# Kernel tuning notes

Hardware: AMD Instinct MI355X
Metric: run time of the kernel (lower is better)

The kernel has to match this reference:

```python
import jax, jax.numpy as jnp
import numpy as np

B, D, H0, H1, O = 4096, 1024, 1024, 1024, 1024  # O = output_dim + 1
ALPHA = 0.3
CLAMP = 0.3


def setup_inputs() -> dict:
    key = jax.random.key(0)
    ks = jax.random.split(key, 15)
    def he(k, fan_in, shape):
        return jax.random.normal(k, shape, dtype=jnp.float32) * np.sqrt(2.0 / fan_in).astype(np.float32)
    def heb(k, shape):
        return jax.random.uniform(k, shape, dtype=jnp.float32, minval=-CLAMP, maxval=CLAMP)
    return {
        "x": jax.random.normal(ks[0], (B, D), dtype=jnp.float32),
        "x2h0": he(ks[1], D, (D, H0)),
        "x2h1": he(ks[2], D, (D, H1)),
        "h02h1": he(ks[3], H0, (H0, H1)),
        "x2y": he(ks[4], D, (D, O)),
        "h02y": he(ks[5], H0, (H0, O)),
        "h12y": he(ks[6], H1, (H1, O)),
        "heb_x2h0": heb(ks[7], (D, H0)),
        "heb_x2h1": heb(ks[8], (D, H1)),
        "heb_h02h1": heb(ks[9], (H0, H1)),
        "heb_x2y": heb(ks[10], (D, O)),
        "heb_h02y": heb(ks[11], (H0, O)),
        "heb_h12y": heb(ks[12], (H1, O)),
        "W": jax.random.uniform(ks[13], (1, 1), dtype=jnp.float32),
    }


def reference(x, x2h0, x2h1, h02h1, x2y, h02y, h12y,
              heb_x2h0, heb_x2h1, heb_h02h1, heb_x2y, heb_h02y, heb_h12y, W):
    clamp = lambda m: jnp.clip(m, -CLAMP, CLAMP)
    # x -> h0
    h0_x = x @ (x2h0 + W * heb_x2h0)                       # [B, H0]
    heb_x2h0_n = clamp(heb_x2h0 + ALPHA * (x.T @ h0_x))
    h0 = jax.nn.relu(h0_x)
    # x -> h1, h0 -> h1
    h1_x = x @ (x2h1 + W * heb_x2h1)                       # [B, H1]
    heb_x2h1_n = clamp(heb_x2h1 + ALPHA * (x.T @ h1_x))
    h1_0 = h0 @ (h02h1 + W * heb_h02h1)
    heb_h02h1_n = clamp(heb_h02h1 + ALPHA * (h0.T @ h1_0))
    h1 = jax.nn.relu(h1_x + h1_0)
    # x, h0, h1 -> y
    y_x = x @ (x2y + W * heb_x2y)                          # [B, O]
    heb_x2y_n = clamp(heb_x2y + ALPHA * (x.T @ y_x))
    y_0 = h0 @ (h02y + W * heb_h02y)
    heb_h02y_n = clamp(heb_h02y + ALPHA * (h0.T @ y_0))
    y_1 = h1 @ (h12y + W * heb_h12y)
    heb_h12y_n = clamp(heb_h12y + ALPHA * (h1.T @ y_1))
    y = y_x + y_0 + y_1
    W_new = jnp.mean(jnp.tanh(y[:, -2:-1]))               # neuromodulator scalar
    dopa = jnp.mean(jnp.tanh(y[:, -3:-2]))
    y_out = y[:, :-2]                                      # [B, O-2]
    return (y_out, heb_x2h0_n, heb_x2h1_n, heb_h02h1_n,
            heb_x2y_n, heb_h02y_n, heb_h12y_n, W_new, dopa)
```

## Files before the change

### kernel.cpp

```cpp
#include <hip/hip_runtime.h>
#include <stdint.h>

#define ALPHA 0.3f
#define CLAMPV 0.3f
#define BDIM 4096
#define NDIM 1024

typedef float f32x4 __attribute__((ext_vector_type(4)));
typedef __bf16 bf16x8 __attribute__((ext_vector_type(8)));

union U16x8 { uint4 v; unsigned short u[8]; };

__device__ __forceinline__ float bf2f(unsigned short u) {
  union { unsigned int i; float f; } c; c.i = ((unsigned int)u) << 16; return c.f;
}
__device__ __forceinline__ unsigned short f2bf(float f) {
  union { float f; unsigned int i; } c; c.f = f;
  unsigned int u = c.i;
  unsigned int r = u + 0x7FFFu + ((u >> 16) & 1u);
  return (unsigned short)(r >> 16);
}

__global__ __launch_bounds__(256) void fill_k(float* __restrict__ out, int n) {
  int i = blockIdx.x * 256 + threadIdx.x;
  if (i < n) out[i] = 12345.0f;
}

__global__ __launch_bounds__(256) void split_x_k(const float* __restrict__ x,
                                                 unsigned short* __restrict__ hi,
                                                 unsigned short* __restrict__ lo) {
  const size_t i0 = ((size_t)blockIdx.x * 256 + threadIdx.x) * 8;
  f32x4 a = *(const f32x4*)(x + i0);
  f32x4 b = *(const f32x4*)(x + i0 + 4);
  U16x8 h8, l8;
#pragma unroll
  for (int i = 0; i < 4; ++i) {
    unsigned short h = f2bf(a[i]); h8.u[i] = h; l8.u[i] = f2bf(a[i] - bf2f(h));
    unsigned short h2 = f2bf(b[i]); h8.u[4+i] = h2; l8.u[4+i] = f2bf(b[i] - bf2f(h2));
  }
  *(uint4*)(hi + i0) = h8.v;
  *(uint4*)(lo + i0) = l8.v;
}

struct TDesc {
  const void* in1; const void* in2; const float* Wp;
  unsigned short* out_hi; unsigned short* out_lo;
  int R, C, tilesC, mode;
};
struct TBatch { TDesc d[8]; int start[9]; int n; };

__global__ __launch_bounds__(256) void transpose_k(TBatch batch) {
  const int bid = blockIdx.x;
  int g = 0;
#pragma unroll
  for (int i = 1; i < 8; ++i)
    if (i < batch.n && bid >= batch.start[i]) g = i;
  TDesc D = batch.d[g];
  const int lt = bid - batch.start[g];
  const int trow = lt / D.tilesC;
  const int tcol = lt - trow * D.tilesC;
  const int r0 = trow * 64, c0 = tcol * 64;

  __shared__ float tile[64][65];
  const int t = threadIdx.x;
  const int sub = t >> 3, oct = t & 7;
  const float Wv = (D.mode == 2) ? *D.Wp : 0.f;

#pragma unroll
  for (int p = 0; p < 2; ++p) {
    const int rl = p * 32 + sub;
    const int cl0 = oct * 8;
    float vv[8];
    if (D.mode == 0) {
      const unsigned short* ip = (const unsigned short*)D.in1 + (size_t)(r0 + rl) * D.C + c0 + cl0;
      U16x8 tmp; tmp.v = *(const uint4*)ip;
#pragma unroll
      for (int i = 0; i < 8; ++i) vv[i] = bf2f(tmp.u[i]);
    } else {
      const float* ip = (const float*)D.in1 + (size_t)(r0 + rl) * D.C + c0 + cl0;
      f32x4 a = *(const f32x4*)ip, b = *(const f32x4*)(ip + 4);
#pragma unroll
      for (int i = 0; i < 4; ++i) { vv[i] = a[i]; vv[4+i] = b[i]; }
      if (D.mode == 2) {
        const float* ip2 = (const float*)D.in2 + (size_t)(r0 + rl) * D.C + c0 + cl0;
        f32x4 c = *(const f32x4*)ip2, d2 = *(const f32x4*)(ip2 + 4);
#pragma unroll
        for (int i = 0; i < 4; ++i) { vv[i] += Wv * c[i]; vv[4+i] += Wv * d2[i]; }
      }
    }
#pragma unroll
    for (int i = 0; i < 8; ++i) tile[cl0 + i][rl] = vv[i];
  }
  __syncthreads();
#pragma unroll
  for (int p = 0; p < 2; ++p) {
    const int cl = p * 32 + sub;
    const int rl0 = oct * 8;
    U16x8 h8, l8;
#pragma unroll
    for (int i = 0; i < 8; ++i) {
      float v = tile[cl][rl0 + i];
      unsigned short h = f2bf(v);
      h8.u[i] = h;
      l8.u[i] = f2bf(v - bf2f(h));
    }
    const size_t o = (size_t)(c0 + cl) * D.R + r0 + rl0;
    *(uint4*)(D.out_hi + o) = h8.v;
    if (D.mode != 0) *(uint4*)(D.out_lo + o) = l8.v;
  }
}

struct GemmDesc {
  const unsigned short *Ahi, *Alo, *Bhi, *Blo;
  int lda, ldb, nk, accadd;
  float* out32a;
  float* out32b;
  const float* addin;
  unsigned short* sp_hi;
  unsigned short* sp_lo;
  const float* heb_in;
  float* heb_out;
};
struct GemmBatch { GemmDesc d[16]; int start[17]; int n; };

#define AS1 __attribute__((address_space(1)))
#define AS3 __attribute__((address_space(3)))

__global__ __launch_bounds__(256, 2) void gemm_k(GemmBatch batch) {
  const int bid = blockIdx.x;
  int g = 0;
#pragma unroll
  for (int i = 1; i < 16; ++i)
    if (i < batch.n && bid >= batch.start[i]) g = i;
  GemmDesc D = batch.d[g];
  const int local = bid - batch.start[g];
  const int tm = local >> 3;
  const int tn = local & 7;

  __shared__ __align__(16) unsigned short LDS[32768];

  const int t = threadIdx.x;
  const int lane = t & 63;
  const int wave = t >> 6;
  const int wr = wave >> 1, wc = wave & 1;
  const int fr = lane & 15, fg = lane >> 4;

  f32x4 acc[8][4];
#pragma unroll
  for (int i = 0; i < 8; ++i)
#pragma unroll
    for (int j = 0; j < 4; ++j)
#pragma unroll
      for (int rr = 0; rr < 4; ++rr) acc[i][j][rr] = 0.f;

  const int r0 = t >> 2;
  const int colSwE = (((t & 3) ^ ((t >> 3) & 3)) << 3);

  size_t aRow[4], bRow[2];
#pragma unroll
  for (int qq = 0; qq < 4; ++qq)
    aRow[qq] = (size_t)(tm * 256 + qq * 64 + r0) * D.lda + colSwE;
#pragma unroll
  for (int qq = 0; qq < 2; ++qq)
    bRow[qq] = (size_t)(tn * 128 + qq * 64 + r0) * D.ldb + colSwE;

  const int ldsW = wave * 512;

  auto stageA = [&](const unsigned short* P, int kb, int b) {
    unsigned short* base = LDS + b * 16384 + ldsW;
#pragma unroll
    for (int qq = 0; qq < 4; ++qq)
      __builtin_amdgcn_global_load_lds(
          (const AS1 void*)(P + aRow[qq] + kb),
          (AS3 void*)(base + qq * 2048), 16, 0, 0);
  };
  auto stageB = [&](const unsigned short* P, int region, int kb, int b) {
    unsigned short* base = LDS + b * 16384 + region + ldsW;
#pragma unroll
    for (int qq = 0; qq < 2; ++qq)
      __builtin_amdgcn_global_load_lds(
          (const AS1 void*)(P + bRow[qq] + kb),
          (AS3 void*)(base + qq * 2048), 16, 0, 0);
  };

  const int swz = ((fg ^ ((fr >> 1) & 3)) << 4);
  int aoff[8], boff[4];
#pragma unroll
  for (int i = 0; i < 8; ++i)
    aoff[i] = (wr * 128 + i * 16 + fr) * 64 + swz;
#pragma unroll
  for (int j = 0; j < 4; ++j)
    boff[j] = 16384 + (wc * 64 + j * 16 + fr) * 64 + swz;
  const char* ldsc = (const char*)LDS;

  auto computePh0 = [&](int b) {
    const char* bb = ldsc + b * 32768;
    bf16x8 af[8];
#pragma unroll
    for (int i = 0; i < 8; ++i) af[i] = *(const bf16x8*)(bb + aoff[i]);
#pragma unroll
    for (int j = 0; j < 4; ++j) {
      const bf16x8 bh = *(const bf16x8*)(bb + boff[j]);
#pragma unroll
      for (int i = 0; i < 8; ++i)
        acc[i][j] = __builtin_amdgcn_mfma_f32_16x16x32_bf16(af[i], bh, acc[i][j], 0, 0, 0);
      const bf16x8 bl = *(const bf16x8*)(bb + boff[j] + 8192);
#pragma unroll
      for (int i = 0; i < 8; ++i)
        acc[i][j] = __builtin_amdgcn_mfma_f32_16x16x32_bf16(af[i], bl, acc[i][j], 0, 0, 0);
    }
  };
  auto computePh1 = [&](int b) {
    const char* bb = ldsc + b * 32768;
    bf16x8 af[8];
#pragma unroll
    for (int i = 0; i < 8; ++i) af[i] = *(const bf16x8*)(bb + aoff[i]);
#pragma unroll
    for (int j = 0; j < 4; ++j) {
      const bf16x8 bh = *(const bf16x8*)(bb + boff[j]);
#pragma unroll
      for (int i = 0; i < 8; ++i)
        acc[i][j] = __builtin_amdgcn_mfma_f32_16x16x32_bf16(af[i], bh, acc[i][j], 0, 0, 0);
    }
  };

  const int n = D.nk;

  stageA(D.Ahi, 0, 0);
  stageB(D.Bhi, 8192, 0, 0);
  stageB(D.Blo, 12288, 0, 0);
  int buf = 0;

#pragma unroll 1
  for (int kt = 0; kt < n; ++kt) {
    if (kt + 1 < n) {
      const int kb = (kt + 1) << 5;
      stageA(D.Ahi, kb, buf ^ 1);
      stageB(D.Bhi, 8192, kb, buf ^ 1);
      stageB(D.Blo, 12288, kb, buf ^ 1);
      asm volatile("s_waitcnt vmcnt(8)" ::: "memory");
    } else {
      stageA(D.Alo, 0, buf ^ 1);
      stageB(D.Bhi, 8192, 0, buf ^ 1);
      asm volatile("s_waitcnt vmcnt(6)" ::: "memory");
    }
    __builtin_amdgcn_s_barrier();
    __builtin_amdgcn_sched_barrier(0);
    computePh0(buf);
    __builtin_amdgcn_sched_barrier(0);
    __builtin_amdgcn_s_barrier();
    buf ^= 1;
  }

#pragma unroll 1
  for (int kt = 0; kt < n; ++kt) {
    if (kt + 1 < n) {
      const int kb = (kt + 1) << 5;
      stageA(D.Alo, kb, buf ^ 1);
      stageB(D.Bhi, 8192, kb, buf ^ 1);
      asm volatile("s_waitcnt vmcnt(6)" ::: "memory");
    } else {
      asm volatile("s_waitcnt vmcnt(0)" ::: "memory");
    }
    __builtin_amdgcn_s_barrier();
    __builtin_amdgcn_sched_barrier(0);
    computePh1(buf);
    __builtin_amdgcn_sched_barrier(0);
    __builtin_amdgcn_s_barrier();
    buf ^= 1;
  }

  const int grb = tm * 256 + wr * 128 + fg * 4;
  const int gcb = tn * 128 + wc * 64 + fr;
#pragma unroll
  for (int i = 0; i < 8; ++i) {
#pragma unroll
    for (int j = 0; j < 4; ++j) {
      const int gc = gcb + j * 16;
#pragma unroll
      for (int rr = 0; rr < 4; ++rr) {
        const int gr = grb + i * 16 + rr;
        const size_t idx = (size_t)gr * NDIM + gc;
        const float v = acc[i][j][rr];
        if (D.heb_out) {
          D.heb_out[idx] = fminf(fmaxf(D.heb_in[idx] + ALPHA * v, -CLAMPV), CLAMPV);
        } else {
          if (D.out32a) D.out32a[idx] = v;
          if (D.out32b) D.out32b[idx] = D.accadd ? (D.out32b[idx] + v) : v;
          if (D.sp_hi) {
            float rv = v + (D.addin ? D.addin[idx] : 0.f);
            rv = fmaxf(rv, 0.f);
            const unsigned short h = f2bf(rv);
            D.sp_hi[idx] = h;
            D.sp_lo[idx] = f2bf(rv - bf2f(h));
          }
        }
      }
    }
  }
}

struct HebRed { const float* heb_in; float* out; const float* p[16]; int np; };

__global__ __launch_bounds__(256) void hebred_k(HebRed R) {
  const size_t i0 = ((size_t)blockIdx.x * 256 + threadIdx.x) * 4;
  f32x4 s = *(const f32x4*)(R.p[0] + i0);
#pragma unroll
  for (int k = 1; k < 16; ++k)
    if (k < R.np) s += *(const f32x4*)(R.p[k] + i0);
  f32x4 h = *(const f32x4*)(R.heb_in + i0);
  f32x4 o;
#pragma unroll
  for (int i = 0; i < 4; ++i) o[i] = fminf(fmaxf(h[i] + ALPHA * s[i], -CLAMPV), CLAMPV);
  *(f32x4*)(R.out + i0) = o;
}

__global__ __launch_bounds__(256) void yassm_k(const float* __restrict__ ysum,
                                               float* __restrict__ yout) {
  const int stride = gridDim.x * 256;
  for (int idx = blockIdx.x * 256 + threadIdx.x; idx < BDIM * 1022; idx += stride) {
    const int row = idx / 1022;
    const int col = idx - row * 1022;
    yout[idx] = ysum[(size_t)row * NDIM + col];
  }
}

__global__ __launch_bounds__(256) void tanhcol_k(const float* __restrict__ ysum,
                                                 float* __restrict__ wpart,
                                                 float* __restrict__ dpart) {
  const int r = blockIdx.x * 256 + threadIdx.x;
  const size_t b = (size_t)r * NDIM;
  float tw = tanhf(ysum[b + 1022]);
  float td = tanhf(ysum[b + 1021]);
#pragma unroll
  for (int o = 32; o > 0; o >>= 1) { tw += __shfl_down(tw, o); td += __shfl_down(td, o); }
  __shared__ float s1[4], s2[4];
  const int lane = threadIdx.x & 63, wv = threadIdx.x >> 6;
  if (lane == 0) { s1[wv] = tw; s2[wv] = td; }
  __syncthreads();
  if (threadIdx.x == 0) {
    wpart[blockIdx.x] = s1[0] + s1[1] + s1[2] + s1[3];
    dpart[blockIdx.x] = s2[0] + s2[1] + s2[2] + s2[3];
  }
}

__global__ void finalize_k(const float* __restrict__ wpart, const float* __restrict__ dpart,
                           float* __restrict__ out, int nout) {
  if (threadIdx.x == 0 && blockIdx.x == 0) {
    float s = 0.f, d = 0.f;
    for (int i = 0; i < 16; ++i) { s += wpart[i]; d += dpart[i]; }
    out[nout - 2] = s * (1.f / BDIM);
    out[nout - 1] = d * (1.f / BDIM);
  }
}

extern "C" void kernel_launch(void* const* d_in, const int* in_sizes, int n_in,
                              void* d_out, int out_size, void* d_ws, size_t ws_size,
                              hipStream_t stream) {
  const float* x = (const float*)d_in[0];
  const float* wbase[6]; const float* hebin[6];
  for (int i = 0; i < 6; ++i) { wbase[i] = (const float*)d_in[1 + i]; hebin[i] = (const float*)d_in[7 + i]; }
  const float* Wp = (const float*)d_in[13];
  float* out = (float*)d_out;
  const size_t YOUT = (size_t)BDIM * 1022;
  float* hebout[6];
  for (int i = 0; i < 6; ++i) hebout[i] = out + YOUT + (size_t)i * 1048576;

  const size_t E = (size_t)BDIM * NDIM;
  const size_t PAIRB = E * 4;
  const size_t WPAIRB = (size_t)NDIM * NDIM * 4;
  const size_t FB = E * 4;
  const size_t REQUIRED = 7 * PAIRB + 6 * WPAIRB + 4 * FB;

  if (ws_size < REQUIRED) {
    fill_k<<<(out_size + 255) / 256, 256, 0, stream>>>(out, out_size);
    return;
  }

  char* p = (char*)d_ws;
  auto takeB = [&](size_t n) -> char* { char* q = p; p += n; return q; };

  unsigned short* R0 = (unsigned short*)takeB(PAIRB);
  unsigned short* R1 = (unsigned short*)takeB(PAIRB);
  unsigned short* R2 = (unsigned short*)takeB(PAIRB);
  unsigned short* R3 = (unsigned short*)takeB(PAIRB);
  unsigned short* R4 = (unsigned short*)takeB(PAIRB);
  unsigned short* R5 = (unsigned short*)takeB(PAIRB);
  unsigned short* R6 = (unsigned short*)takeB(PAIRB);
  unsigned short* WThi[6]; unsigned short* WTlo[6];
  for (int i = 0; i < 6; ++i) {
    WThi[i] = (unsigned short*)takeB(WPAIRB);
    WTlo[i] = WThi[i] + (size_t)NDIM * NDIM;
  }
  float* F0 = (float*)takeB(FB);
  float* F1 = (float*)takeB(FB);
  float* F2 = (float*)takeB(FB);
  float* F3 = (float*)takeB(FB);

  unsigned short *xhi = R0, *xlo = R0 + E;
  unsigned short *xThi = R1, *xTlo = R1 + E;
  unsigned short *h0hi = R2, *h0lo = R2 + E;
  unsigned short *h0Thi = R3, *h0Tlo = R3 + E;
  float* wpart = (float*)R3; float* dpart = wpart + 64;

  split_x_k<<<2048, 256, 0, stream>>>(x, xhi, xlo);

  {
    TBatch tb{};
    int s = 0;
    for (int i = 0; i < 6; ++i) {
      tb.d[i] = { wbase[i], hebin[i], Wp, WThi[i], WTlo[i], NDIM, NDIM, NDIM / 64, 2 };
      tb.start[i] = s; s += (NDIM / 64) * (NDIM / 64);
    }
    tb.d[6] = { x, nullptr, nullptr, xThi, xTlo, BDIM, NDIM, NDIM / 64, 1 };
    tb.start[6] = s; s += (BDIM / 64) * (NDIM / 64);
    tb.start[7] = s; tb.n = 7;
    transpose_k<<<s, 256, 0, stream>>>(tb);
  }

  auto fwdDesc = [&](const unsigned short* ahi, const unsigned short* alo, int wi) -> GemmDesc {
    GemmDesc d{};
    d.Ahi = ahi; d.Alo = alo; d.Bhi = WThi[wi]; d.Blo = WTlo[wi];
    d.lda = NDIM; d.ldb = NDIM; d.nk = NDIM / 32;
    return d;
  };
  auto hebPart = [&](const unsigned short* ahi, const unsigned short* alo,
                     const unsigned short* bhi, const unsigned short* blo,
                     int koff, int klen, float* partOut) -> GemmDesc {
    GemmDesc d{};
    d.Ahi = ahi + koff; d.Alo = alo + koff;
    d.Bhi = bhi + koff; d.Blo = blo + koff;
    d.lda = BDIM; d.ldb = BDIM; d.nk = klen / 32;
    d.out32a = partOut;
    return d;
  };

  {
    GemmBatch gb{};
    gb.d[0] = fwdDesc(xhi, xlo, 0);
    gb.d[0].out32a = F0; gb.d[0].sp_hi = h0hi; gb.d[0].sp_lo = h0lo;
    gb.d[1] = fwdDesc(xhi, xlo, 1);
    gb.d[1].out32a = F1;
    gb.d[2] = fwdDesc(xhi, xlo, 3);
    gb.d[2].out32a = F2; gb.d[2].out32b = F3; gb.d[2].accadd = 0;
    gb.start[0] = 0; gb.start[1] = 128; gb.start[2] = 256; gb.start[3] = 384;
    gb.n = 3;
    gemm_k<<<384, 256, 0, stream>>>(gb);
  }

  {
    TBatch tb{};
    tb.d[0] = { F0, nullptr, nullptr, R4, R4 + E, BDIM, NDIM, NDIM / 64, 1 };
    tb.d[1] = { F1, nullptr, nullptr, R5, R5 + E, BDIM, NDIM, NDIM / 64, 1 };
    tb.d[2] = { F2, nullptr, nullptr, R6, R6 + E, BDIM, NDIM, NDIM / 64, 1 };
    tb.d[3] = { h0hi, nullptr, nullptr, h0Thi, nullptr, BDIM, NDIM, NDIM / 64, 0 };
    tb.d[4] = { h0lo, nullptr, nullptr, h0Tlo, nullptr, BDIM, NDIM, NDIM / 64, 0 };
    for (int i = 0; i < 6; ++i) tb.start[i] = i * 1024;
    tb.n = 5;
    transpose_k<<<5120, 256, 0, stream>>>(tb);
  }

  {
    float* px0a = (float*)WThi[0]; float* px0b = hebout[0];
    float* px1a = (float*)WThi[1]; float* px1b = hebout[1];
    float* pxya = (float*)WThi[3]; float* pxyb = hebout[3];
    GemmBatch gb{};
    gb.d[0] = hebPart(xThi, xTlo, R4, R4 + E, 0,    2048, px0a);
    gb.d[1] = hebPart(xThi, xTlo, R4, R4 + E, 2048, 2048, px0b);
    gb.d[2] = hebPart(xThi, xTlo, R5, R5 + E, 0,    2048, px1a);
    gb.d[3] = hebPart(xThi, xTlo, R5, R5 + E, 2048, 2048, px1b);
    gb.d[4] = hebPart(xThi, xTlo, R6, R6 + E, 0,    2048, pxya);
    gb.d[5] = hebPart(xThi, xTlo, R6, R6 + E, 2048, 2048, pxyb);
    gb.d[6] = fwdDesc(h0hi, h0lo, 2);
    gb.d[6].out32a = F0; gb.d[6].addin = F1; gb.d[6].sp_hi = R0; gb.d[6].sp_lo = R0 + E;
    gb.d[7] = fwdDesc(h0hi, h0lo, 4);
    gb.d[7].out32a = F2; gb.d[7].out32b = F3; gb.d[7].accadd = 1;
    for (int i = 0; i < 6; ++i) gb.start[i] = i * 32;
    gb.start[6] = 192; gb.start[7] = 320; gb.start[8] = 448;
    gb.n = 8;
    gemm_k<<<448, 256, 0, stream>>>(gb);
    HebRed r0x{}; r0x.heb_in = hebin[0]; r0x.out = hebout[0]; r0x.p[0]=px0a; r0x.p[1]=px0b; r0x.np=2;
    hebred_k<<<1024, 256, 0, stream>>>(r0x);
    HebRed r1x{}; r1x.heb_in = hebin[1]; r1x.out = hebout[1]; r1x.p[0]=px1a; r1x.p[1]=px1b; r1x.np=2;
    hebred_k<<<1024, 256, 0, stream>>>(r1x);
    HebRed ryx{}; ryx.heb_in = hebin[3]; ryx.out = hebout[3]; ryx.p[0]=pxya; ryx.p[1]=pxyb; ryx.np=2;
    hebred_k<<<1024, 256, 0, stream>>>(ryx);
  }

  {
    TBatch tb{};
    tb.d[0] = { F0, nullptr, nullptr, R4, R4 + E, BDIM, NDIM, NDIM / 64, 1 };
    tb.d[1] = { F2, nullptr, nullptr, R5, R5 + E, BDIM, NDIM, NDIM / 64, 1 };
    tb.d[2] = { R0, nullptr, nullptr, R1, nullptr, BDIM, NDIM, NDIM / 64, 0 };
    tb.d[3] = { R0 + E, nullptr, nullptr, R1 + E, nullptr, BDIM, NDIM, NDIM / 64, 0 };
    for (int i = 0; i < 5; ++i) tb.start[i] = i * 1024;
    tb.n = 4;
    transpose_k<<<4096, 256, 0, stream>>>(tb);
  }

  {
    float* pa[4] = { (float*)WThi[0], (float*)WThi[1], (float*)WThi[2], (float*)WThi[3] };
    float* pb[4] = { (float*)R6, (float*)R6 + 1048576, (float*)R6 + 2097152, (float*)R6 + 3145728 };
    GemmBatch gb{};
    for (int h = 0; h < 4; ++h) {
      gb.d[h]     = hebPart(h0Thi, h0Tlo, R4, R4 + E, h * 1024, 1024, pa[h]);
      gb.d[4 + h] = hebPart(h0Thi, h0Tlo, R5, R5 + E, h * 1024, 1024, pb[h]);
    }
    gb.d[8] = fwdDesc(R0, R0 + E, 5);
    gb.d[8].out32a = F1; gb.d[8].out32b = F3; gb.d[8].accadd = 1;
    for (int i = 0; i < 8; ++i) gb.start[i] = i * 32;
    gb.start[8] = 256; gb.start[9] = 384;
    gb.n = 9;
    gemm_k<<<384, 256, 0, stream>>>(gb);
    HebRed rh{}; rh.heb_in = hebin[2]; rh.out = hebout[2];
    for (int h = 0; h < 4; ++h) rh.p[h] = pa[h];
    rh.np = 4;
    hebred_k<<<1024, 256, 0, stream>>>(rh);
    HebRed ry{}; ry.heb_in = hebin[4]; ry.out = hebout[4];
    for (int h = 0; h < 4; ++h) ry.p[h] = pb[h];
    ry.np = 4;
    hebred_k<<<1024, 256, 0, stream>>>(ry);
  }

  {
    TBatch tb{};
    tb.d[0] = { F1, nullptr, nullptr, R2, R2 + E, BDIM, NDIM, NDIM / 64, 1 };
    tb.start[0] = 0; tb.start[1] = 1024; tb.n = 1;
    transpose_k<<<1024, 256, 0, stream>>>(tb);
  }

  {
    float* parts[16];
    for (int h = 0; h < 4; ++h) {
      parts[h]      = (float*)R4 + (size_t)h * 1048576;
      parts[4 + h]  = (float*)R5 + (size_t)h * 1048576;
      parts[8 + h]  = (float*)R6 + (size_t)h * 1048576;
      parts[12 + h] = (float*)WThi[h];
    }
    GemmBatch gb{};
    for (int h = 0; h < 16; ++h)
      gb.d[h] = hebPart(R1, R1 + E, R2, R2 + E, h * 256, 256, parts[h]);
    for (int i = 0; i <= 16; ++i) gb.start[i] = i * 32;
    gb.n = 16;
    gemm_k<<<512, 256, 0, stream>>>(gb);
    HebRed rf{}; rf.heb_in = hebin[5]; rf.out = hebout[5];
    for (int h = 0; h < 16; ++h) rf.p[h] = parts[h];
    rf.np = 16;
    hebred_k<<<1024, 256, 0, stream>>>(rf);
  }

  yassm_k<<<2048, 256, 0, stream>>>(F3, out);
  tanhcol_k<<<16, 256, 0, stream>>>(F3, wpart, dpart);
  finalize_k<<<1, 64, 0, stream>>>(wpart, dpart, out, out_size);
}
```

Before: 523.8 us.

## Fuse transposed bf16 split outputs into GEMM epilogue and batch heb reductions

The GEMM epilogue now writes transposed hi/lo bf16 splits of the raw and relu'd results straight to workspace, replacing separate fp32 intermediate stores and most standalone transpose kernels. The heb reduction launches are merged into batched kernels indexed by block id. Together these remove fp32 round-trips through global memory and several kernel launches. The cost is strided 8-byte transposed stores from the epilogue, which coalesce poorly, plus a reshuffled workspace layout that has to stay alias-safe.

New measurement: 551.9 us. +5.4%, slower.

```diff
diff --git a/kernel.cpp b/kernel.cpp
--- a/kernel.cpp
+++ b/kernel.cpp
@@ -10,6 +10,7 @@
 typedef __bf16 bf16x8 __attribute__((ext_vector_type(8)));
 
 union U16x8 { uint4 v; unsigned short u[8]; };
+union U16x4 { uint2 v; unsigned short u[4]; };
 
 __device__ __forceinline__ float bf2f(unsigned short u) {
   union { unsigned int i; float f; } c; c.i = ((unsigned int)u) << 16; return c.f;
@@ -118,8 +119,10 @@
   const float* addin;
   unsigned short* sp_hi;
   unsigned short* sp_lo;
-  const float* heb_in;
-  float* heb_out;
+  unsigned short* tr_hi;
+  unsigned short* tr_lo;
+  unsigned short* spT_hi;
+  unsigned short* spT_lo;
 };
 struct GemmBatch { GemmDesc d[16]; int start[17]; int n; };
 
@@ -274,45 +277,68 @@
   const int gcb = tn * 128 + wc * 64 + fr;
 #pragma unroll
   for (int i = 0; i < 8; ++i) {
+    const int gr0 = grb + i * 16;
 #pragma unroll
     for (int j = 0; j < 4; ++j) {
       const int gc = gcb + j * 16;
+      const f32x4 v = acc[i][j];
+      f32x4 rv;
 #pragma unroll
       for (int rr = 0; rr < 4; ++rr) {
-        const int gr = grb + i * 16 + rr;
-        const size_t idx = (size_t)gr * NDIM + gc;
-        const float v = acc[i][j][rr];
-        if (D.heb_out) {
-          D.heb_out[idx] = fminf(fmaxf(D.heb_in[idx] + ALPHA * v, -CLAMPV), CLAMPV);
-        } else {
-          if (D.out32a) D.out32a[idx] = v;
-          if (D.out32b) D.out32b[idx] = D.accadd ? (D.out32b[idx] + v) : v;
-          if (D.sp_hi) {
-            float rv = v + (D.addin ? D.addin[idx] : 0.f);
-            rv = fmaxf(rv, 0.f);
-            const unsigned short h = f2bf(rv);
-            D.sp_hi[idx] = h;
-            D.sp_lo[idx] = f2bf(rv - bf2f(h));
-          }
+        const size_t idx = (size_t)(gr0 + rr) * NDIM + gc;
+        if (D.out32a) D.out32a[idx] = v[rr];
+        if (D.out32b) D.out32b[idx] = D.accadd ? (D.out32b[idx] + v[rr]) : v[rr];
+        const float tsum = v[rr] + (D.addin ? D.addin[idx] : 0.f);
+        rv[rr] = fmaxf(tsum, 0.f);
+        if (D.sp_hi) {
+          const unsigned short h = f2bf(rv[rr]);
+          D.sp_hi[idx] = h;
+          D.sp_lo[idx] = f2bf(rv[rr] - bf2f(h));
         }
       }
-    }
-  }
-}
-
-struct HebRed { const float* heb_in; float* out; const float* p[16]; int np; };
-
-__global__ __launch_bounds__(256) void hebred_k(HebRed R) {
-  const size_t i0 = ((size_t)blockIdx.x * 256 + threadIdx.x) * 4;
-  f32x4 s = *(const f32x4*)(R.p[0] + i0);
+      const size_t tb = (size_t)gc * BDIM + gr0;
+      if (D.tr_hi) {
+        U16x4 h2, l2;
+#pragma unroll
+        for (int rr = 0; rr < 4; ++rr) {
+          const unsigned short h = f2bf(v[rr]);
+          h2.u[rr] = h; l2.u[rr] = f2bf(v[rr] - bf2f(h));
+        }
+        *(uint2*)(D.tr_hi + tb) = h2.v;
+        *(uint2*)(D.tr_lo + tb) = l2.v;
+      }
+      if (D.spT_hi) {
+        U16x4 h2, l2;
+#pragma unroll
+        for (int rr = 0; rr < 4; ++rr) {
+          const unsigned short h = f2bf(rv[rr]);
+          h2.u[rr] = h; l2.u[rr] = f2bf(rv[rr] - bf2f(h));
+        }
+        *(uint2*)(D.spT_hi + tb) = h2.v;
+        *(uint2*)(D.spT_lo + tb) = l2.v;
+      }
+    }
+  }
+}
+
+struct HebRedB {
+  const float* heb_in[3]; float* outp[3];
+  const float* p[3][16]; int np[3]; int n;
+};
+
+__global__ __launch_bounds__(256) void hebred_k(HebRedB B) {
+  const int g = blockIdx.x >> 10;
+  const int local = blockIdx.x & 1023;
+  const size_t i0 = ((size_t)local * 256 + threadIdx.x) * 4;
+  f32x4 s = *(const f32x4*)(B.p[g][0] + i0);
 #pragma unroll
   for (int k = 1; k < 16; ++k)
-    if (k < R.np) s += *(const f32x4*)(R.p[k] + i0);
-  f32x4 h = *(const f32x4*)(R.heb_in + i0);
+    if (k < B.np[g]) s += *(const f32x4*)(B.p[g][k] + i0);
+  f32x4 h = *(const f32x4*)(B.heb_in[g] + i0);
   f32x4 o;
 #pragma unroll
   for (int i = 0; i < 4; ++i) o[i] = fminf(fmaxf(h[i] + ALPHA * s[i], -CLAMPV), CLAMPV);
-  *(f32x4*)(R.out + i0) = o;
+  *(f32x4*)(B.outp[g] + i0) = o;
 }
 
 __global__ __launch_bounds__(256) void yassm_k(const float* __restrict__ ysum,
@@ -370,7 +396,7 @@
   const size_t PAIRB = E * 4;
   const size_t WPAIRB = (size_t)NDIM * NDIM * 4;
   const size_t FB = E * 4;
-  const size_t REQUIRED = 7 * PAIRB + 6 * WPAIRB + 4 * FB;
+  const size_t REQUIRED = 9 * PAIRB + 6 * WPAIRB + 2 * FB;
 
   if (ws_size < REQUIRED) {
     fill_k<<<(out_size + 255) / 256, 256, 0, stream>>>(out, out_size);
@@ -380,28 +406,28 @@
   char* p = (char*)d_ws;
   auto takeB = [&](size_t n) -> char* { char* q = p; p += n; return q; };
 
-  unsigned short* R0 = (unsigned short*)takeB(PAIRB);
-  unsigned short* R1 = (unsigned short*)takeB(PAIRB);
-  unsigned short* R2 = (unsigned short*)takeB(PAIRB);
-  unsigned short* R3 = (unsigned short*)takeB(PAIRB);
-  unsigned short* R4 = (unsigned short*)takeB(PAIRB);
-  unsigned short* R5 = (unsigned short*)takeB(PAIRB);
-  unsigned short* R6 = (unsigned short*)takeB(PAIRB);
+  unsigned short* P0 = (unsigned short*)takeB(PAIRB);
+  unsigned short* P1 = (unsigned short*)takeB(PAIRB);
+  unsigned short* P2 = (unsigned short*)takeB(PAIRB);
+  unsigned short* P3 = (unsigned short*)takeB(PAIRB);
+  unsigned short* P4 = (unsigned short*)takeB(PAIRB);
+  unsigned short* P5 = (unsigned short*)takeB(PAIRB);
+  unsigned short* P6 = (unsigned short*)takeB(PAIRB);
+  unsigned short* P7 = (unsigned short*)takeB(PAIRB);
+  unsigned short* P8 = (unsigned short*)takeB(PAIRB);
   unsigned short* WThi[6]; unsigned short* WTlo[6];
   for (int i = 0; i < 6; ++i) {
     WThi[i] = (unsigned short*)takeB(WPAIRB);
     WTlo[i] = WThi[i] + (size_t)NDIM * NDIM;
   }
-  float* F0 = (float*)takeB(FB);
   float* F1 = (float*)takeB(FB);
-  float* F2 = (float*)takeB(FB);
   float* F3 = (float*)takeB(FB);
 
-  unsigned short *xhi = R0, *xlo = R0 + E;
-  unsigned short *xThi = R1, *xTlo = R1 + E;
-  unsigned short *h0hi = R2, *h0lo = R2 + E;
-  unsigned short *h0Thi = R3, *h0Tlo = R3 + E;
-  float* wpart = (float*)R3; float* dpart = wpart + 64;
+  unsigned short *xhi = P0, *xlo = P0 + E;
+  unsigned short *xThi = P1, *xTlo = P1 + E;
+  unsigned short *h0hi = P2, *h0lo = P2 + E;
+  unsigned short *h0Thi = P3, *h0Tlo = P3 + E;
+  float* wpart = (float*)P8; float* dpart = wpart + 64;
 
   split_x_k<<<2048, 256, 0, stream>>>(x, xhi, xlo);
 
@@ -438,26 +464,18 @@
   {
     GemmBatch gb{};
     gb.d[0] = fwdDesc(xhi, xlo, 0);
-    gb.d[0].out32a = F0; gb.d[0].sp_hi = h0hi; gb.d[0].sp_lo = h0lo;
+    gb.d[0].sp_hi = h0hi; gb.d[0].sp_lo = h0lo;
+    gb.d[0].tr_hi = P4; gb.d[0].tr_lo = P4 + E;
+    gb.d[0].spT_hi = h0Thi; gb.d[0].spT_lo = h0Tlo;
     gb.d[1] = fwdDesc(xhi, xlo, 1);
     gb.d[1].out32a = F1;
+    gb.d[1].tr_hi = P5; gb.d[1].tr_lo = P5 + E;
     gb.d[2] = fwdDesc(xhi, xlo, 3);
-    gb.d[2].out32a = F2; gb.d[2].out32b = F3; gb.d[2].accadd = 0;
+    gb.d[2].out32b = F3; gb.d[2].accadd = 0;
+    gb.d[2].tr_hi = P6; gb.d[2].tr_lo = P6 + E;
     gb.start[0] = 0; gb.start[1] = 128; gb.start[2] = 256; gb.start[3] = 384;
     gb.n = 3;
     gemm_k<<<384, 256, 0, stream>>>(gb);
-  }
-
-  {
-    TBatch tb{};
-    tb.d[0] = { F0, nullptr, nullptr, R4, R4 + E, BDIM, NDIM, NDIM / 64, 1 };
-    tb.d[1] = { F1, nullptr, nullptr, R5, R5 + E, BDIM, NDIM, NDIM / 64, 1 };
-    tb.d[2] = { F2, nullptr, nullptr, R6, R6 + E, BDIM, NDIM, NDIM / 64, 1 };
-    tb.d[3] = { h0hi, nullptr, nullptr, h0Thi, nullptr, BDIM, NDIM, NDIM / 64, 0 };
-    tb.d[4] = { h0lo, nullptr, nullptr, h0Tlo, nullptr, BDIM, NDIM, NDIM / 64, 0 };
-    for (int i = 0; i < 6; ++i) tb.start[i] = i * 1024;
-    tb.n = 5;
-    transpose_k<<<5120, 256, 0, stream>>>(tb);
   }
 
   {
@@ -465,88 +483,85 @@
     float* px1a = (float*)WThi[1]; float* px1b = hebout[1];
     float* pxya = (float*)WThi[3]; float* pxyb = hebout[3];
     GemmBatch gb{};
-    gb.d[0] = hebPart(xThi, xTlo, R4, R4 + E, 0,    2048, px0a);
-    gb.d[1] = hebPart(xThi, xTlo, R4, R4 + E, 2048, 2048, px0b);
-    gb.d[2] = hebPart(xThi, xTlo, R5, R5 + E, 0,    2048, px1a);
-    gb.d[3] = hebPart(xThi, xTlo, R5, R5 + E, 2048, 2048, px1b);
-    gb.d[4] = hebPart(xThi, xTlo, R6, R6 + E, 0,    2048, pxya);
-    gb.d[5] = hebPart(xThi, xTlo, R6, R6 + E, 2048, 2048, pxyb);
+    gb.d[0] = hebPart(xThi, xTlo, P4, P4 + E, 0,    2048, px0a);
+    gb.d[1] = hebPart(xThi, xTlo, P4, P4 + E, 2048, 2048, px0b);
+    gb.d[2] = hebPart(xThi, xTlo, P5, P5 + E, 0,    2048, px1a);
+    gb.d[3] = hebPart(xThi, xTlo, P5, P5 + E, 2048, 2048, px1b);
+    gb.d[4] = hebPart(xThi, xTlo, P6, P6 + E, 0,    2048, pxya);
+    gb.d[5] = hebPart(xThi, xTlo, P6, P6 + E, 2048, 2048, pxyb);
     gb.d[6] = fwdDesc(h0hi, h0lo, 2);
-    gb.d[6].out32a = F0; gb.d[6].addin = F1; gb.d[6].sp_hi = R0; gb.d[6].sp_lo = R0 + E;
+    gb.d[6].addin = F1;
+    gb.d[6].sp_hi = P0; gb.d[6].sp_lo = P0 + E;
+    gb.d[6].tr_hi = P7; gb.d[6].tr_lo = P7 + E;
     gb.d[7] = fwdDesc(h0hi, h0lo, 4);
-    gb.d[7].out32a = F2; gb.d[7].out32b = F3; gb.d[7].accadd = 1;
+    gb.d[7].out32b = F3; gb.d[7].accadd = 1;
+    gb.d[7].tr_hi = P8; gb.d[7].tr_lo = P8 + E;
     for (int i = 0; i < 6; ++i) gb.start[i] = i * 32;
     gb.start[6] = 192; gb.start[7] = 320; gb.start[8] = 448;
     gb.n = 8;
     gemm_k<<<448, 256, 0, stream>>>(gb);
-    HebRed r0x{}; r0x.heb_in = hebin[0]; r0x.out = hebout[0]; r0x.p[0]=px0a; r0x.p[1]=px0b; r0x.np=2;
-    hebred_k<<<1024, 256, 0, stream>>>(r0x);
-    HebRed r1x{}; r1x.heb_in = hebin[1]; r1x.out = hebout[1]; r1x.p[0]=px1a; r1x.p[1]=px1b; r1x.np=2;
-    hebred_k<<<1024, 256, 0, stream>>>(r1x);
-    HebRed ryx{}; ryx.heb_in = hebin[3]; ryx.out = hebout[3]; ryx.p[0]=pxya; ryx.p[1]=pxyb; ryx.np=2;
-    hebred_k<<<1024, 256, 0, stream>>>(ryx);
+    HebRedB rb{};
+    rb.heb_in[0] = hebin[0]; rb.outp[0] = hebout[0]; rb.p[0][0] = px0a; rb.p[0][1] = px0b; rb.np[0] = 2;
+    rb.heb_in[1] = hebin[1]; rb.outp[1] = hebout[1]; rb.p[1][0] = px1a; rb.p[1][1] = px1b; rb.np[1] = 2;
+    rb.heb_in[2] = hebin[3]; rb.outp[2] = hebout[3]; rb.p[2][0] = pxya; rb.p[2][1] = pxyb; rb.np[2] = 2;
+    rb.n = 3;
+    hebred_k<<<3072, 256, 0, stream>>>(rb);
   }
 
   {
     TBatch tb{};
-    tb.d[0] = { F0, nullptr, nullptr, R4, R4 + E, BDIM, NDIM, NDIM / 64, 1 };
-    tb.d[1] = { F2, nullptr, nullptr, R5, R5 + E, BDIM, NDIM, NDIM / 64, 1 };
-    tb.d[2] = { R0, nullptr, nullptr, R1, nullptr, BDIM, NDIM, NDIM / 64, 0 };
-    tb.d[3] = { R0 + E, nullptr, nullptr, R1 + E, nullptr, BDIM, NDIM, NDIM / 64, 0 };
-    for (int i = 0; i < 5; ++i) tb.start[i] = i * 1024;
-    tb.n = 4;
-    transpose_k<<<4096, 256, 0, stream>>>(tb);
+    tb.d[0] = { P0,     nullptr, nullptr, P4,     nullptr, BDIM, NDIM, NDIM / 64, 0 };
+    tb.d[1] = { P0 + E, nullptr, nullptr, P4 + E, nullptr, BDIM, NDIM, NDIM / 64, 0 };
+    tb.start[0] = 0; tb.start[1] = 1024; tb.start[2] = 2048; tb.n = 2;
+    transpose_k<<<2048, 256, 0, stream>>>(tb);
   }
 
   {
-    float* pa[4] = { (float*)WThi[0], (float*)WThi[1], (float*)WThi[2], (float*)WThi[3] };
-    float* pb[4] = { (float*)R6, (float*)R6 + 1048576, (float*)R6 + 2097152, (float*)R6 + 3145728 };
+    float* pa[4] = { (float*)WThi[0], (float*)WThi[1], (float*)WThi[2], hebout[2] };
+    float* pb[4] = { (float*)WThi[3], (float*)WThi[4], (float*)P2, hebout[4] };
     GemmBatch gb{};
     for (int h = 0; h < 4; ++h) {
-      gb.d[h]     = hebPart(h0Thi, h0Tlo, R4, R4 + E, h * 1024, 1024, pa[h]);
-      gb.d[4 + h] = hebPart(h0Thi, h0Tlo, R5, R5 + E, h * 1024, 1024, pb[h]);
-    }
-    gb.d[8] = fwdDesc(R0, R0 + E, 5);
-    gb.d[8].out32a = F1; gb.d[8].out32b = F3; gb.d[8].accadd = 1;
+      gb.d[h]     = hebPart(h0Thi, h0Tlo, P7, P7 + E, h * 1024, 1024, pa[h]);
+      gb.d[4 + h] = hebPart(h0Thi, h0Tlo, P8, P8 + E, h * 1024, 1024, pb[h]);
+    }
+    gb.d[8] = fwdDesc(P0, P0 + E, 5);
+    gb.d[8].out32b = F3; gb.d[8].accadd = 1;
+    gb.d[8].tr_hi = P5; gb.d[8].tr_lo = P5 + E;
     for (int i = 0; i < 8; ++i) gb.start[i] = i * 32;
     gb.start[8] = 256; gb.start[9] = 384;
     gb.n = 9;
     gemm_k<<<384, 256, 0, stream>>>(gb);
-    HebRed rh{}; rh.heb_in = hebin[2]; rh.out = hebout[2];
-    for (int h = 0; h < 4; ++h) rh.p[h] = pa[h];
-    rh.np = 4;
-    hebred_k<<<1024, 256, 0, stream>>>(rh);
-    HebRed ry{}; ry.heb_in = hebin[4]; ry.out = hebout[4];
-    for (int h = 0; h < 4; ++h) ry.p[h] = pb[h];
-    ry.np = 4;
-    hebred_k<<<1024, 256, 0, stream>>>(ry);
-  }
-
-  {
-    TBatch tb{};
-    tb.d[0] = { F1, nullptr, nullptr, R2, R2 + E, BDIM, NDIM, NDIM / 64, 1 };
-    tb.start[0] = 0; tb.start[1] = 1024; tb.n = 1;
-    transpose_k<<<1024, 256, 0, stream>>>(tb);
+    HebRedB rb{};
+    rb.heb_in[0] = hebin[2]; rb.outp[0] = hebout[2];
+    for (int h = 0; h < 4; ++h) rb.p[0][h] = pa[h];
+    rb.np[0] = 4;
+    rb.heb_in[1] = hebin[4]; rb.outp[1] = hebout[4];
+    for (int h = 0; h < 4; ++h) rb.p[1][h] = pb[h];
+    rb.np[1] = 4;
+    rb.n = 2;
+    hebred_k<<<2048, 256, 0, stream>>>(rb);
   }
 
   {
     float* parts[16];
     for (int h = 0; h < 4; ++h) {
-      parts[h]      = (float*)R4 + (size_t)h * 1048576;
-      parts[4 + h]  = (float*)R5 + (size_t)h * 1048576;
-      parts[8 + h]  = (float*)R6 + (size_t)h * 1048576;
-      parts[12 + h] = (float*)WThi[h];
+      parts[h]      = (float*)P2 + (size_t)h * 1048576;
+      parts[4 + h]  = (float*)P3 + (size_t)h * 1048576;
+      parts[8 + h]  = (float*)P6 + (size_t)h * 1048576;
+      parts[12 + h] = (float*)P7 + (size_t)h * 1048576;
     }
     GemmBatch gb{};
     for (int h = 0; h < 16; ++h)
-      gb.d[h] = hebPart(R1, R1 + E, R2, R2 + E, h * 256, 256, parts[h]);
+      gb.d[h] = hebPart(P4, P4 + E, P5, P5 + E, h * 256, 256, parts[h]);
     for (int i = 0; i <= 16; ++i) gb.start[i] = i * 32;
     gb.n = 16;
     gemm_k<<<512, 256, 0, stream>>>(gb);
-    HebRed rf{}; rf.heb_in = hebin[5]; rf.out = hebout[5];
-    for (int h = 0; h < 16; ++h) rf.p[h] = parts[h];
-    rf.np = 16;
-    hebred_k<<<1024, 256, 0, stream>>>(rf);
+    HebRedB rb{};
+    rb.heb_in[0] = hebin[5]; rb.outp[0] = hebout[5];
+    for (int h = 0; h < 16; ++h) rb.p[0][h] = parts[h];
+    rb.np[0] = 16;
+    rb.n = 1;
+    hebred_k<<<1024, 256, 0, stream>>>(rb);
   }
 
   yassm_k<<<2048, 256, 0, stream>>>(F3, out);
```
